# Kernel optimization log

Measured on AMD Instinct MI355X. Metric: run time of the kernel, lower is better.

The kernel has to match this reference:

```python
import jax, jax.numpy as jnp
import numpy as np

N = 100000      # nodes
E = 3200000     # edges (avg degree 32)
F_IN = 500      # input features
HID = 8         # per-head hidden dim (layer 1)
HEADS = 8       # heads (layer 1)
NC = 41         # num classes (layer 2, 1 head)


def setup_inputs() -> dict:
    key = jax.random.key(0)
    ks = jax.random.split(key, 8)
    x = jax.random.normal(ks[0], (N, F_IN), jnp.float32)
    edge_index = jax.random.randint(ks[1], (2, E), 0, N, dtype=jnp.int64)
    W1 = jax.random.normal(ks[2], (F_IN, HEADS * HID), jnp.float32) / np.sqrt(F_IN)
    a1_src = jax.random.normal(ks[3], (HEADS, HID), jnp.float32) / np.sqrt(HID)
    a1_dst = jax.random.normal(ks[4], (HEADS, HID), jnp.float32) / np.sqrt(HID)
    W2 = jax.random.normal(ks[5], (HEADS * HID, NC), jnp.float32) / np.sqrt(HEADS * HID)
    a2_src = jax.random.normal(ks[6], (1, NC), jnp.float32) / np.sqrt(NC)
    a2_dst = jax.random.normal(ks[7], (1, NC), jnp.float32) / np.sqrt(NC)
    return {"x": x, "edge_index": edge_index, "W1": W1, "a1_src": a1_src,
            "a1_dst": a1_dst, "W2": W2, "a2_src": a2_src, "a2_dst": a2_dst}


def gat_layer(x, edge_index, W, a_src, a_dst, heads, out_dim, concat):
    n = x.shape[0]
    h = (x @ W).reshape(n, heads, out_dim)                    # [N,H,D]
    # per-node attention halves (avoids gathering full features for logits)
    alpha_src = jnp.einsum('nhd,hd->nh', h, a_src)            # [N,H]
    alpha_dst = jnp.einsum('nhd,hd->nh', h, a_dst)            # [N,H]
    src, dst = edge_index[0], edge_index[1]
    e = jax.nn.leaky_relu(alpha_src[src] + alpha_dst[dst], 0.2)  # [E,H]
    # segment softmax over incoming edges of each destination node
    e_max = jax.lax.stop_gradient(jax.ops.segment_max(e, dst, num_segments=n))
    e_exp = jnp.exp(e - e_max[dst])
    denom = jax.ops.segment_sum(e_exp, dst, num_segments=n)
    alpha = e_exp / (denom[dst] + 1e-16)                      # [E,H]
    msg = alpha[:, :, None] * h[src]                          # [E,H,D]
    out = jax.ops.segment_sum(msg, dst, num_segments=n)       # [N,H,D]
    return out.reshape(n, heads * out_dim) if concat else out.mean(axis=1)


def reference(x, edge_index, W1, a1_src, a1_dst, W2, a2_src, a2_dst):
    # dropout layers are identity at inference
    h = gat_layer(x, edge_index, W1, a1_src, a1_dst, HEADS, HID, True)   # [N,64]
    h = jax.nn.elu(h)
    out = gat_layer(h, edge_index, W2, a2_src, a2_dst, 1, NC, False)     # [N,41]
    return jax.nn.log_softmax(out, axis=1)
```

## Files before the change

kernel.cpp:

```cpp
#include <hip/hip_runtime.h>
#include <hip/hip_bf16.h>
#include <math.h>


#define DEV __device__ __forceinline__

constexpr int N_NODES = 100000;
constexpr int N_EDGES = 3200000;
constexpr int F_IN    = 500;
constexpr int HEADS   = 8;
constexpr int HID     = 8;
constexpr int D1      = HEADS * HID;
constexpr int NC      = 41;
constexpr int NCP     = 64;

constexpr int NB    = 782;
constexpr int BCAP  = 5120;
constexpr int CSTR  = 16;
constexpr int SEPT  = 8;
constexpr int SCHUNK = 512 * SEPT;
constexpr int SBLKS = (N_EDGES + SCHUNK - 1) / SCHUNK;

constexpr int GROWS = 32;
constexpr int LROW  = 520;
constexpr int GBLKS = N_NODES / GROWS;

constexpr int WSTR = 68;

typedef __attribute__((ext_vector_type(8))) short bf16x8;
typedef __attribute__((ext_vector_type(4))) float f32x4;

DEV float bf2f(unsigned short u) {
    return __uint_as_float(((unsigned int)u) << 16);
}
DEV unsigned short f2b(float f) {
    unsigned int u = __float_as_uint(f);
    unsigned int r = (u + 0x7FFFu + ((u >> 16) & 1u)) >> 16;
    return (unsigned short)r;
}
DEV float leaky(float e) { return e > 0.f ? e : 0.2f * e; }
DEV float readlane_f(float v, int l) {
    return __uint_as_float((unsigned int)__builtin_amdgcn_readlane((int)__float_as_uint(v), l));
}

__global__ void k_detect(const void* xraw, const void* eraw, int* flags) {
    const int lane = threadIdx.x & 63;
    const unsigned short* xu = (const unsigned short*)xraw;
    unsigned short v = xu[2 * lane];
    int e = (v >> 7) & 0xFF;
    int valid = (e == 0 || (e >= 90 && e <= 150)) ? 1 : 0;
    unsigned long long vm = __ballot(valid);
    const unsigned int* eu = (const unsigned int*)eraw;
    unsigned long long zm = __ballot(eu[2 * lane + 1] == 0u);
    if (lane == 0) {
        flags[0] = (__popcll(vm) < 56) ? 1 : 0;
        flags[1] = (__popcll(zm) == 64) ? 1 : 0;
    }
}

__global__ __launch_bounds__(256) void k_convert(const void* w1, const void* a1s, const void* a1d,
                                                 const void* w2, const void* a2s, const void* a2d,
                                                 const int* flags,
                                                 unsigned short* W1frag, float* A1Sf, float* A1Df,
                                                 float* W2f, float* A2Sf, float* A2Df) {
    const bool f32 = flags[0] != 0;
    if (blockIdx.x == 0) {
        auto conv = [&](const void* src, float* dst, int n) {
            if (f32) {
                const float* s = (const float*)src;
                for (int i = threadIdx.x; i < n; i += blockDim.x) dst[i] = s[i];
            } else {
                const unsigned short* s = (const unsigned short*)src;
                for (int i = threadIdx.x; i < n; i += blockDim.x) dst[i] = bf2f(s[i]);
            }
        };
        conv(a1s, A1Sf, HEADS * HID);
        conv(a1d, A1Df, HEADS * HID);
        conv(w2, W2f, D1 * NC);
        conv(a2s, A2Sf, NC);
        conv(a2d, A2Df, NC);
    }
    for (int idx = blockIdx.x * 256 + threadIdx.x; idx < 4 * 16 * 64 * 8; idx += 64 * 256) {
        int wid = idx >> 13, kb = (idx >> 9) & 15, ln = (idx >> 3) & 63, j = idx & 7;
        int k = kb * 32 + (ln >> 4) * 8 + j;
        int n = wid * 16 + (ln & 15);
        unsigned short bits = 0;
        if (k < F_IN) {
            if (f32) bits = f2b(((const float*)w1)[k * D1 + n]);
            else     bits = ((const unsigned short*)w1)[k * D1 + n];
        }
        W1frag[idx] = bits;
    }
}

__global__ __launch_bounds__(512, 8) void k_gemm1_scat(const void* xraw, const void* eraw,
                                                       const int* flags,
                                                       const unsigned short* __restrict__ W1frag,
                                                       const float* A1Sf, const float* A1Df,
                                                       unsigned short* __restrict__ h1b,
                                                       float* __restrict__ as1,
                                                       float* __restrict__ ad1,
                                                       int* bucket_cnt, unsigned int* staging) {
    __shared__ unsigned short ldsx[GROWS * LROW];
    const int t = threadIdx.x;

    if (blockIdx.x < SBLKS) {
        int* bh = (int*)ldsx;
        for (int i = t; i < NB; i += 512) bh[i] = 0;
        __syncthreads();
        const bool e64 = flags[1] != 0;
        const unsigned int* eu = (const unsigned int*)eraw;
        const int e0 = blockIdx.x * SCHUNK;
        int sv[SEPT], dv[SEPT];
#pragma unroll
        for (int k = 0; k < SEPT; k++) {
            int i = e0 + k * 512 + t;
            if (i < N_EDGES) {
                if (e64) { sv[k] = (int)eu[2 * i]; dv[k] = (int)eu[2 * (N_EDGES + i)]; }
                else     { sv[k] = (int)eu[i];     dv[k] = (int)eu[N_EDGES + i]; }
                atomicAdd(&bh[dv[k] >> 7], 1);
            } else dv[k] = -1;
        }
        __syncthreads();
        for (int i = t; i < NB; i += 512) {
            int c = bh[i];
            int base = c ? atomicAdd(&bucket_cnt[i * CSTR], c) : 0;
            bh[i] = i * BCAP + base;
        }
        __syncthreads();
#pragma unroll
        for (int k = 0; k < SEPT; k++) {
            if (dv[k] >= 0) {
                int b = dv[k] >> 7;
                int slot = atomicAdd(&bh[b], 1);
                staging[slot] = (unsigned)sv[k] | ((unsigned)(dv[k] & 127) << 17);
            }
        }
        return;
    }

    const int r0 = (blockIdx.x - SBLKS) * GROWS;
    const bool xf32 = flags[0] != 0;
#pragma unroll 4
    for (int it = 0; it < 8; it++) {
        int s = it * 512 + t;
        int row = s >> 7, c4 = s & 127;
        int row_g = r0 + row;
        ushort4 v = make_ushort4(0, 0, 0, 0);
        if (c4 < 125) {
            if (xf32) {
                float4 f = *(const float4*)((const float*)xraw + (size_t)row_g * F_IN + c4 * 4);
                v = make_ushort4(f2b(f.x), f2b(f.y), f2b(f.z), f2b(f.w));
            } else {
                v = *(const ushort4*)((const unsigned short*)xraw + (size_t)row_g * F_IN + c4 * 4);
            }
        }
        *(ushort4*)(ldsx + row * LROW + c4 * 4) = v;
    }
    __syncthreads();

    const int lane = t & 63;
    const int w = t >> 6;
    const int wid = __builtin_amdgcn_readfirstlane(w & 3);
    const int mb  = __builtin_amdgcn_readfirstlane(w >> 2);
    const int m = lane & 15, q = lane >> 4;
    f32x4 acc = {0.f, 0.f, 0.f, 0.f};
    const unsigned short* wf = W1frag + (size_t)wid * 8192;
    const unsigned short* arow = ldsx + (mb * 16 + m) * LROW + q * 8;
#pragma unroll 4
    for (int kb = 0; kb < 16; kb++) {
        bf16x8 b = *(const bf16x8*)(wf + (kb * 64 + lane) * 8);
        bf16x8 a = *(const bf16x8*)(arow + kb * 32);
        acc = __builtin_amdgcn_mfma_f32_16x16x32_bf16(a, b, acc, 0, 0, 0);
    }
    const int col = wid * 16 + m;
    const float a_s = A1Sf[col], a_d = A1Df[col];
    const int h = 2 * wid + (m >> 3);
#pragma unroll
    for (int reg = 0; reg < 4; reg++) {
        int gr = r0 + mb * 16 + q * 4 + reg;
        float vacc = acc[reg];
        h1b[(size_t)gr * D1 + col] = f2b(vacc);
        float ts = vacc * a_s, td = vacc * a_d;
        ts += __shfl_xor(ts, 1, 64); td += __shfl_xor(td, 1, 64);
        ts += __shfl_xor(ts, 2, 64); td += __shfl_xor(td, 2, 64);
        ts += __shfl_xor(ts, 4, 64); td += __shfl_xor(td, 4, 64);
        if ((lane & 7) == 0) {
            as1[gr * HEADS + h] = ts;
            ad1[gr * HEADS + h] = td;
        }
    }
}

__global__ __launch_bounds__(1024) void k_cscan(const int* bucket_cnt, int* cbase, int* off) {
    __shared__ int s[1024];
    int t = threadIdx.x;
    s[t] = (t < NB) ? bucket_cnt[t * CSTR] : 0;
    __syncthreads();
    for (int o = 1; o < 1024; o <<= 1) {
        int v = (t >= o) ? s[t - o] : 0;
        __syncthreads();
        s[t] += v;
        __syncthreads();
    }
    if (t < NB) cbase[t + 1] = s[t];
    if (t == 0) { cbase[0] = 0; off[N_NODES] = N_EDGES; }
}

__global__ __launch_bounds__(256) void k_csr_build(const unsigned int* __restrict__ staging,
                                                   const int* __restrict__ bucket_cnt,
                                                   const int* __restrict__ cbase,
                                                   int* __restrict__ off, int* __restrict__ csr) {
    __shared__ int sdeg[128];
    __shared__ int scur[128];
    const int t = threadIdx.x;
    const int b = blockIdx.x;
    const int n0 = b << 7;
    const int start = b * BCAP;
    const int end = start + bucket_cnt[b * CSTR];
    const int base = cbase[b];
    if (t < 128) sdeg[t] = 0;
    __syncthreads();
    for (int i = start + t; i < end; i += 256)
        atomicAdd(&sdeg[staging[i] >> 17], 1);
    __syncthreads();
    int d = (t < 128) ? sdeg[t] : 0;
    for (int o = 1; o < 128; o <<= 1) {
        int v = (t >= o && t < 128) ? sdeg[t - o] : 0;
        __syncthreads();
        if (t < 128) sdeg[t] += v;
        __syncthreads();
    }
    if (t < 128) {
        int excl = sdeg[t] - d;
        if (n0 + t < N_NODES) off[n0 + t] = base + excl;
        scur[t] = base + excl;
    }
    __syncthreads();
    for (int i = start + t; i < end; i += 256) {
        unsigned v = staging[i];
        int slot = atomicAdd(&scur[v >> 17], 1);
        csr[slot] = (int)(v & 0x1FFFFu);
    }
}

__global__ __launch_bounds__(256) void k_agg1(const int* __restrict__ csr,
                                              const int* __restrict__ off,
                                              const unsigned short* __restrict__ h1b,
                                              const float* __restrict__ as1,
                                              const float* __restrict__ ad1,
                                              float* __restrict__ h1e) {
    __shared__ float wlds[4][8 * WSTR];
    const int t = threadIdx.x;
    const int lane = t & 63;
    const int n = (blockIdx.x * blockDim.x + t) >> 6;
    if (n >= N_NODES) return;
    const int beg = off[n], end = off[n + 1];
    const int h0 = lane >> 3;
    float* wl = wlds[(t >> 6) & 3];
    const float* wrow = wl + h0 * WSTR;
    const float* adp = ad1 + n * HEADS;
    float acc = 0.f, dsum = 0.f;
    for (int base = beg; base < end; base += 64) {
        const int cnt = min(64, end - base);
        int sl = 0;
        if (lane < cnt) {
            sl = csr[base + lane];
            const float* ap = as1 + sl * HEADS;
            float4 aa = *(const float4*)(ap);
            float4 ab = *(const float4*)(ap + 4);
            wl[0 * WSTR + lane] = __expf(leaky(aa.x + adp[0]));
            wl[1 * WSTR + lane] = __expf(leaky(aa.y + adp[1]));
            wl[2 * WSTR + lane] = __expf(leaky(aa.z + adp[2]));
            wl[3 * WSTR + lane] = __expf(leaky(aa.w + adp[3]));
            wl[4 * WSTR + lane] = __expf(leaky(ab.x + adp[4]));
            wl[5 * WSTR + lane] = __expf(leaky(ab.y + adp[5]));
            wl[6 * WSTR + lane] = __expf(leaky(ab.z + adp[6]));
            wl[7 * WSTR + lane] = __expf(leaky(ab.w + adp[7]));
        }
        asm volatile("s_waitcnt lgkmcnt(0)" ::: "memory");
        int j = 0;
        for (; j + 4 <= cnt; j += 4) {
            int s0 = __builtin_amdgcn_readlane(sl, j);
            int s1 = __builtin_amdgcn_readlane(sl, j + 1);
            int s2 = __builtin_amdgcn_readlane(sl, j + 2);
            int s3 = __builtin_amdgcn_readlane(sl, j + 3);
            float4 wv = *(const float4*)(wrow + j);
            float g0 = bf2f(h1b[(size_t)s0 * D1 + lane]);
            float g1 = bf2f(h1b[(size_t)s1 * D1 + lane]);
            float g2 = bf2f(h1b[(size_t)s2 * D1 + lane]);
            float g3 = bf2f(h1b[(size_t)s3 * D1 + lane]);
            acc = fmaf(wv.x, g0, acc); dsum += wv.x;
            acc = fmaf(wv.y, g1, acc); dsum += wv.y;
            acc = fmaf(wv.z, g2, acc); dsum += wv.z;
            acc = fmaf(wv.w, g3, acc); dsum += wv.w;
        }
        for (; j < cnt; j++) {
            int s = __builtin_amdgcn_readlane(sl, j);
            float w = wrow[j];
            acc = fmaf(w, bf2f(h1b[(size_t)s * D1 + lane]), acc);
            dsum += w;
        }
    }
    float v = acc / (dsum + 1e-16f);
    float o = v > 0.f ? v : (__expf(v) - 1.f);
    h1e[(size_t)n * D1 + lane] = o;
}

__global__ __launch_bounds__(256) void k_gemm2(const float* __restrict__ h1e,
                                               const float* __restrict__ W2f,
                                               const float* __restrict__ A2Sf,
                                               const float* __restrict__ A2Df,
                                               unsigned short* __restrict__ h2p,
                                               float* __restrict__ as2,
                                               float* __restrict__ ad2) {
    const int row = blockIdx.x * blockDim.x + threadIdx.x;
    if (row >= N_NODES) return;
    float acc[NC];
#pragma unroll
    for (int c = 0; c < NC; c++) acc[c] = 0.f;
    const float* xr = h1e + (size_t)row * D1;
    for (int k = 0; k < D1; k += 4) {
        float4 hv = *(const float4*)(xr + k);
#pragma unroll
        for (int c = 0; c < NC; c++) {
            acc[c] = fmaf(hv.x, W2f[(k + 0) * NC + c], acc[c]);
            acc[c] = fmaf(hv.y, W2f[(k + 1) * NC + c], acc[c]);
            acc[c] = fmaf(hv.z, W2f[(k + 2) * NC + c], acc[c]);
            acc[c] = fmaf(hv.w, W2f[(k + 3) * NC + c], acc[c]);
        }
    }
    float ts = 0.f, td = 0.f;
#pragma unroll
    for (int c = 0; c < NC; c++) {
        h2p[(size_t)row * NCP + c] = f2b(acc[c]);
        ts = fmaf(acc[c], A2Sf[c], ts);
        td = fmaf(acc[c], A2Df[c], td);
    }
    as2[row] = ts;
    ad2[row] = td;
}

__global__ __launch_bounds__(256) void k_agg2(const int* __restrict__ csr,
                                              const int* __restrict__ off,
                                              const unsigned short* __restrict__ h2p,
                                              const float* __restrict__ as2,
                                              const float* __restrict__ ad2,
                                              const int* flags, void* out) {
    const int lane = threadIdx.x & 63;
    const int n = (blockIdx.x * blockDim.x + threadIdx.x) >> 6;
    if (n >= N_NODES) return;
    const int beg = off[n], end = off[n + 1];
    const float ad = ad2[n];
    const bool act = lane < NC;
    const int cl = act ? lane : 0;
    float acc = 0.f, dsum = 0.f;
    for (int base = beg; base < end; base += 64) {
        const int cnt = min(64, end - base);
        int idx = min(base + lane, N_EDGES - 1);
        int sl = csr[idx];
        float w = __expf(leaky(as2[sl] + ad));
        int j = 0;
        for (; j + 4 <= cnt; j += 4) {
            int s0 = __builtin_amdgcn_readlane(sl, j);
            int s1 = __builtin_amdgcn_readlane(sl, j + 1);
            int s2 = __builtin_amdgcn_readlane(sl, j + 2);
            int s3 = __builtin_amdgcn_readlane(sl, j + 3);
            float w0 = readlane_f(w, j);
            float w1 = readlane_f(w, j + 1);
            float w2 = readlane_f(w, j + 2);
            float w3 = readlane_f(w, j + 3);
            float g0 = bf2f(h2p[(size_t)s0 * NCP + cl]);
            float g1 = bf2f(h2p[(size_t)s1 * NCP + cl]);
            float g2 = bf2f(h2p[(size_t)s2 * NCP + cl]);
            float g3 = bf2f(h2p[(size_t)s3 * NCP + cl]);
            acc = fmaf(w0, g0, acc); dsum += w0;
            acc = fmaf(w1, g1, acc); dsum += w1;
            acc = fmaf(w2, g2, acc); dsum += w2;
            acc = fmaf(w3, g3, acc); dsum += w3;
        }
        for (; j < cnt; j++) {
            int s = __builtin_amdgcn_readlane(sl, j);
            float wj = readlane_f(w, j);
            acc = fmaf(wj, bf2f(h2p[(size_t)s * NCP + cl]), acc);
            dsum += wj;
        }
    }
    float val = acc / (dsum + 1e-16f);
    float v = act ? val : -INFINITY;
    float m = v;
#pragma unroll
    for (int o = 1; o < 64; o <<= 1) m = fmaxf(m, __shfl_xor(m, o, 64));
    float ex = act ? __expf(val - m) : 0.f;
#pragma unroll
    for (int o = 1; o < 64; o <<= 1) ex += __shfl_xor(ex, o, 64);
    float res = val - m - __logf(ex);
    if (act) {
        if (flags[0])
            ((float*)out)[(size_t)n * NC + lane] = res;
        else
            ((__hip_bfloat16*)out)[(size_t)n * NC + lane] = __float2bfloat16(res);
    }
}

extern "C" void kernel_launch(void* const* d_in, const int* in_sizes, int n_in,
                              void* d_out, int out_size, void* d_ws, size_t ws_size,
                              hipStream_t stream) {
    char* p = (char*)d_ws;
    auto alloc = [&](size_t bytes) -> void* {
        void* r = (void*)p;
        p += (bytes + 255) & ~(size_t)255;
        return r;
    };
    int* flags  = (int*)alloc(16);
    unsigned short* W1frag = (unsigned short*)alloc(4 * 16 * 64 * 8 * 2);
    float* A1Sf = (float*)alloc(HEADS * HID * 4);
    float* A1Df = (float*)alloc(HEADS * HID * 4);
    float* W2f  = (float*)alloc((size_t)D1 * NC * 4);
    float* A2Sf = (float*)alloc(NC * 4);
    float* A2Df = (float*)alloc(NC * 4);
    unsigned short* h1b = (unsigned short*)alloc((size_t)N_NODES * D1 * 2);
    float* as1  = (float*)alloc((size_t)N_NODES * HEADS * 4);
    float* ad1  = (float*)alloc((size_t)N_NODES * HEADS * 4);
    float* h1e  = (float*)alloc((size_t)N_NODES * D1 * 4);
    unsigned short* h2p = (unsigned short*)alloc((size_t)N_NODES * NCP * 2);
    float* as2  = (float*)alloc((size_t)N_NODES * 4);
    float* ad2  = (float*)alloc((size_t)N_NODES * 4);
    int* off    = (int*)alloc((size_t)(N_NODES + 1) * 4);
    int* csr    = (int*)alloc((size_t)N_EDGES * 4);
    int* bucket_cnt = (int*)alloc((size_t)NB * CSTR * 4);
    int* cbase      = (int*)alloc((size_t)(NB + 1) * 4);
    unsigned int* staging = (unsigned int*)h1e;

    hipMemsetAsync(bucket_cnt, 0, (size_t)NB * CSTR * 4, stream);

    k_detect<<<1, 64, 0, stream>>>(d_in[0], d_in[1], flags);
    k_convert<<<64, 256, 0, stream>>>(d_in[2], d_in[3], d_in[4], d_in[5], d_in[6], d_in[7],
                                      flags, W1frag, A1Sf, A1Df, W2f, A2Sf, A2Df);
    k_gemm1_scat<<<SBLKS + GBLKS, 512, 0, stream>>>(d_in[0], d_in[1], flags, W1frag,
                                                    A1Sf, A1Df, h1b, as1, ad1,
                                                    bucket_cnt, staging);
    k_cscan<<<1, 1024, 0, stream>>>(bucket_cnt, cbase, off);
    k_csr_build<<<NB, 256, 0, stream>>>(staging, bucket_cnt, cbase, off, csr);

    k_agg1<<<25000, 256, 0, stream>>>(csr, off, h1b, as1, ad1, h1e);
    k_gemm2<<<391, 256, 0, stream>>>(h1e, W2f, A2Sf, A2Df, h2p, as2, ad2);
    k_agg2<<<25000, 256, 0, stream>>>(csr, off, h2p, as2, ad2, flags, d_out);
}
```

Baseline: 623.0 us.

## Replace bucketed two-level CSR build with global degree count, scan and scatter

The CSR construction changes from a bucketed staging approach (LDS histogram per 128-node bucket, then a per-bucket local sort) to a classic count/scan/scatter. Degrees come from global atomics fused into the GEMM1 launch, three small kernels do a multi-block prefix scan, and a scatter kernel re-reads the edge list and places each source with a global atomic on a per-node cursor. This removes the staging buffer and the per-bucket pass, but adds 6.4M global atomics with random addresses, a second read of the edge list, and extra kernel launches. Neighbor order within a node becomes nondeterministic.

```diff
diff --git a/kernel.cpp b/kernel.cpp
--- a/kernel.cpp
+++ b/kernel.cpp
@@ -14,12 +14,11 @@
 constexpr int NC      = 41;
 constexpr int NCP     = 64;
 
-constexpr int NB    = 782;
-constexpr int BCAP  = 5120;
-constexpr int CSTR  = 16;
 constexpr int SEPT  = 8;
 constexpr int SCHUNK = 512 * SEPT;
-constexpr int SBLKS = (N_EDGES + SCHUNK - 1) / SCHUNK;
+constexpr int EBLKS = (N_EDGES + SCHUNK - 1) / SCHUNK;
+
+constexpr int SCBLK = (N_NODES + 1023) / 1024;
 
 constexpr int GROWS = 32;
 constexpr int LROW  = 520;
@@ -93,53 +92,33 @@
     }
 }
 
-__global__ __launch_bounds__(512, 8) void k_gemm1_scat(const void* xraw, const void* eraw,
-                                                       const int* flags,
-                                                       const unsigned short* __restrict__ W1frag,
-                                                       const float* A1Sf, const float* A1Df,
-                                                       unsigned short* __restrict__ h1b,
-                                                       float* __restrict__ as1,
-                                                       float* __restrict__ ad1,
-                                                       int* bucket_cnt, unsigned int* staging) {
+__global__ __launch_bounds__(512, 8) void k_gemm1_deg(const void* xraw, const void* eraw,
+                                                      const int* flags,
+                                                      const unsigned short* __restrict__ W1frag,
+                                                      const float* A1Sf, const float* A1Df,
+                                                      unsigned short* __restrict__ h1b,
+                                                      float* __restrict__ as1,
+                                                      float* __restrict__ ad1,
+                                                      int* __restrict__ deg) {
     __shared__ unsigned short ldsx[GROWS * LROW];
     const int t = threadIdx.x;
 
-    if (blockIdx.x < SBLKS) {
-        int* bh = (int*)ldsx;
-        for (int i = t; i < NB; i += 512) bh[i] = 0;
-        __syncthreads();
+    if (blockIdx.x < EBLKS) {
         const bool e64 = flags[1] != 0;
         const unsigned int* eu = (const unsigned int*)eraw;
         const int e0 = blockIdx.x * SCHUNK;
-        int sv[SEPT], dv[SEPT];
 #pragma unroll
         for (int k = 0; k < SEPT; k++) {
             int i = e0 + k * 512 + t;
             if (i < N_EDGES) {
-                if (e64) { sv[k] = (int)eu[2 * i]; dv[k] = (int)eu[2 * (N_EDGES + i)]; }
-                else     { sv[k] = (int)eu[i];     dv[k] = (int)eu[N_EDGES + i]; }
-                atomicAdd(&bh[dv[k] >> 7], 1);
-            } else dv[k] = -1;
-        }
-        __syncthreads();
-        for (int i = t; i < NB; i += 512) {
-            int c = bh[i];
-            int base = c ? atomicAdd(&bucket_cnt[i * CSTR], c) : 0;
-            bh[i] = i * BCAP + base;
-        }
-        __syncthreads();
-#pragma unroll
-        for (int k = 0; k < SEPT; k++) {
-            if (dv[k] >= 0) {
-                int b = dv[k] >> 7;
-                int slot = atomicAdd(&bh[b], 1);
-                staging[slot] = (unsigned)sv[k] | ((unsigned)(dv[k] & 127) << 17);
+                int d = e64 ? (int)eu[2 * (N_EDGES + i)] : (int)eu[N_EDGES + i];
+                atomicAdd(&deg[d], 1);
             }
         }
         return;
     }
 
-    const int r0 = (blockIdx.x - SBLKS) * GROWS;
+    const int r0 = (blockIdx.x - EBLKS) * GROWS;
     const bool xf32 = flags[0] != 0;
 #pragma unroll 4
     for (int it = 0; it < 8; it++) {
@@ -192,10 +171,13 @@
     }
 }
 
-__global__ __launch_bounds__(1024) void k_cscan(const int* bucket_cnt, int* cbase, int* off) {
+__global__ __launch_bounds__(1024) void k_scan1(const int* __restrict__ deg,
+                                                int* __restrict__ off, int* __restrict__ bsum) {
     __shared__ int s[1024];
-    int t = threadIdx.x;
-    s[t] = (t < NB) ? bucket_cnt[t * CSTR] : 0;
+    const int t = threadIdx.x;
+    const int n = blockIdx.x * 1024 + t;
+    int d = (n < N_NODES) ? deg[n] : 0;
+    s[t] = d;
     __syncthreads();
     for (int o = 1; o < 1024; o <<= 1) {
         int v = (t >= o) ? s[t - o] : 0;
@@ -203,44 +185,55 @@
         s[t] += v;
         __syncthreads();
     }
-    if (t < NB) cbase[t + 1] = s[t];
-    if (t == 0) { cbase[0] = 0; off[N_NODES] = N_EDGES; }
-}
-
-__global__ __launch_bounds__(256) void k_csr_build(const unsigned int* __restrict__ staging,
-                                                   const int* __restrict__ bucket_cnt,
-                                                   const int* __restrict__ cbase,
-                                                   int* __restrict__ off, int* __restrict__ csr) {
-    __shared__ int sdeg[128];
-    __shared__ int scur[128];
-    const int t = threadIdx.x;
-    const int b = blockIdx.x;
-    const int n0 = b << 7;
-    const int start = b * BCAP;
-    const int end = start + bucket_cnt[b * CSTR];
-    const int base = cbase[b];
-    if (t < 128) sdeg[t] = 0;
+    if (n < N_NODES) off[n] = s[t] - d;
+    if (t == 1023) bsum[blockIdx.x] = s[1023];
+}
+
+__global__ __launch_bounds__(128) void k_scan2(const int* __restrict__ bsum,
+                                               int* __restrict__ bpre) {
+    __shared__ int s[128];
+    const int t = threadIdx.x;
+    int d = (t < SCBLK) ? bsum[t] : 0;
+    s[t] = d;
     __syncthreads();
-    for (int i = start + t; i < end; i += 256)
-        atomicAdd(&sdeg[staging[i] >> 17], 1);
-    __syncthreads();
-    int d = (t < 128) ? sdeg[t] : 0;
     for (int o = 1; o < 128; o <<= 1) {
-        int v = (t >= o && t < 128) ? sdeg[t - o] : 0;
+        int v = (t >= o) ? s[t - o] : 0;
         __syncthreads();
-        if (t < 128) sdeg[t] += v;
+        s[t] += v;
         __syncthreads();
     }
-    if (t < 128) {
-        int excl = sdeg[t] - d;
-        if (n0 + t < N_NODES) off[n0 + t] = base + excl;
-        scur[t] = base + excl;
-    }
-    __syncthreads();
-    for (int i = start + t; i < end; i += 256) {
-        unsigned v = staging[i];
-        int slot = atomicAdd(&scur[v >> 17], 1);
-        csr[slot] = (int)(v & 0x1FFFFu);
+    if (t < SCBLK) bpre[t] = s[t] - d;
+}
+
+__global__ __launch_bounds__(1024) void k_scan3(int* __restrict__ off,
+                                                const int* __restrict__ bpre,
+                                                int* __restrict__ cur) {
+    const int t = threadIdx.x;
+    const int n = blockIdx.x * 1024 + t;
+    if (n < N_NODES) {
+        int o = off[n] + bpre[blockIdx.x];
+        off[n] = o;
+        cur[n] = o;
+    }
+    if (n == 0) off[N_NODES] = N_EDGES;
+}
+
+__global__ __launch_bounds__(512) void k_scatter(const void* eraw, const int* flags,
+                                                 int* __restrict__ cur, int* __restrict__ csr) {
+    const int t = threadIdx.x;
+    const bool e64 = flags[1] != 0;
+    const unsigned int* eu = (const unsigned int*)eraw;
+    const int e0 = blockIdx.x * SCHUNK;
+#pragma unroll
+    for (int k = 0; k < SEPT; k++) {
+        int i = e0 + k * 512 + t;
+        if (i < N_EDGES) {
+            int s, d;
+            if (e64) { s = (int)eu[2 * i]; d = (int)eu[2 * (N_EDGES + i)]; }
+            else     { s = (int)eu[i];     d = (int)eu[N_EDGES + i]; }
+            int slot = atomicAdd(&cur[d], 1);
+            csr[slot] = s;
+        }
     }
 }
 
@@ -428,20 +421,22 @@
     float* ad2  = (float*)alloc((size_t)N_NODES * 4);
     int* off    = (int*)alloc((size_t)(N_NODES + 1) * 4);
     int* csr    = (int*)alloc((size_t)N_EDGES * 4);
-    int* bucket_cnt = (int*)alloc((size_t)NB * CSTR * 4);
-    int* cbase      = (int*)alloc((size_t)(NB + 1) * 4);
-    unsigned int* staging = (unsigned int*)h1e;
-
-    hipMemsetAsync(bucket_cnt, 0, (size_t)NB * CSTR * 4, stream);
+    int* deg    = (int*)alloc((size_t)N_NODES * 4);
+    int* cur    = (int*)alloc((size_t)N_NODES * 4);
+    int* bsum   = (int*)alloc((size_t)SCBLK * 4);
+    int* bpre   = (int*)alloc((size_t)SCBLK * 4);
+
+    hipMemsetAsync(deg, 0, (size_t)N_NODES * 4, stream);
 
     k_detect<<<1, 64, 0, stream>>>(d_in[0], d_in[1], flags);
     k_convert<<<64, 256, 0, stream>>>(d_in[2], d_in[3], d_in[4], d_in[5], d_in[6], d_in[7],
                                       flags, W1frag, A1Sf, A1Df, W2f, A2Sf, A2Df);
-    k_gemm1_scat<<<SBLKS + GBLKS, 512, 0, stream>>>(d_in[0], d_in[1], flags, W1frag,
-                                                    A1Sf, A1Df, h1b, as1, ad1,
-                                                    bucket_cnt, staging);
-    k_cscan<<<1, 1024, 0, stream>>>(bucket_cnt, cbase, off);
-    k_csr_build<<<NB, 256, 0, stream>>>(staging, bucket_cnt, cbase, off, csr);
+    k_gemm1_deg<<<EBLKS + GBLKS, 512, 0, stream>>>(d_in[0], d_in[1], flags, W1frag,
+                                                   A1Sf, A1Df, h1b, as1, ad1, deg);
+    k_scan1<<<SCBLK, 1024, 0, stream>>>(deg, off, bsum);
+    k_scan2<<<1, 128, 0, stream>>>(bsum, bpre);
+    k_scan3<<<SCBLK, 1024, 0, stream>>>(off, bpre, cur);
+    k_scatter<<<EBLKS, 512, 0, stream>>>(d_in[1], flags, cur, csr);
 
     k_agg1<<<25000, 256, 0, stream>>>(csr, off, h1b, as1, ad1, h1e);
     k_gemm2<<<391, 256, 0, stream>>>(h1e, W2f, A2Sf, A2Df, h2p, as2, ad2);
```

After: 932.5 us. 1.5x slower.
